# Kernel optimization log

Hardware: AMD Instinct MI355X
Metric: run time of the kernel (lower is better)

The kernel has to match this reference:

```python
import jax, jax.numpy as jnp
import numpy as np

TAU = 0.5      # init kwarg tau
LAMBD = 0.5    # init kwarg lambd
N, D, C = 4096, 1024, 512


def setup_inputs() -> dict:
    key = jax.random.key(0)
    k1, k2, k3 = jax.random.split(key, 3)
    return {
        "layer_embeds": jax.random.normal(k1, (N, D), dtype=jnp.float32),
        "y_true": jax.random.randint(k2, (N,), 0, C),
        "y_pred": jax.random.normal(k3, (N, C), dtype=jnp.float32),
    }


def _clce(x, y_true, y_pred):
    n = x.shape[0]
    # pairwise cosine similarity via one matmul (torch eps = 1e-8)
    norms = jnp.clip(jnp.linalg.norm(x, axis=1, keepdims=True), 1e-8)
    xn = x / norms
    sim = (xn @ xn.T + 1.0) * 0.5 * TAU          # [N, N]

    same = y_true[:, None] == y_true[None, :]    # diagonal is always True
    eye = jnp.eye(n, dtype=bool)
    pos_mask = same & ~eye                        # candidate positives (j != i)
    neg_mask = ~same                              # negatives (excludes diagonal)

    # slot 0: similarity to the FIRST positive j (in j order), else stays 0
    first_pos = jnp.argmax(pos_mask, axis=1)
    has_pos = pos_mask.any(axis=1)
    slot0 = jnp.where(has_pos,
                      jnp.take_along_axis(sim, first_pos[:, None], axis=1)[:, 0],
                      0.0)

    # negatives packed left-to-right into columns 1..; unfilled slots stay 0
    cum = jnp.cumsum(neg_mask, axis=1)            # 1-based slot per negative
    cols = jnp.where(neg_mask, cum, 2 * n - 1)    # non-negatives -> sink col
    rows = jnp.arange(n)[:, None]
    loss_temp = jnp.zeros((n, 2 * n), dtype=sim.dtype)
    loss_temp = loss_temp.at[rows, cols].add(jnp.where(neg_mask, sim, 0.0))
    loss_temp = loss_temp.at[:, 0].set(slot0)
    loss_temp = loss_temp[:, : 2 * n - 1]         # drop sink column -> [N, 2N-1]

    cl = -jax.nn.log_softmax(loss_temp, axis=1)[:, 0]
    cl = cl.sum() / n

    logp = jax.nn.log_softmax(y_pred, axis=1)
    ce = -jnp.take_along_axis(logp, y_true[:, None], axis=1).mean()

    return LAMBD * cl + (1.0 - LAMBD) * ce


def reference(layer_embeds, y_true, y_pred):
    return _clce(layer_embeds, y_true, y_pred)
```

## Files before the change

### kernel.cpp

```cpp
#include <hip/hip_runtime.h>
#include <hip/hip_bf16.h>

#define NR 4096
#define DIM 1024
#define NCLS 512

typedef __attribute__((ext_vector_type(4))) float f32x4;
typedef __attribute__((ext_vector_type(8))) short bf16x8;

static __device__ __forceinline__ unsigned short f2bf(float f) {
  __hip_bfloat16 h = __float2bfloat16(f);
  return *reinterpret_cast<unsigned short*>(&h);
}

__global__ __launch_bounds__(256) void k_prep(const float* __restrict__ x,
                                              const int* __restrict__ y,
                                              const float* __restrict__ yp,
                                              unsigned short* __restrict__ xn,
                                              int* __restrict__ cnt,
                                              int* __restrict__ fpos,
                                              float* __restrict__ slot0,
                                              float* __restrict__ ce,
                                              float* __restrict__ out) {
  const int b = blockIdx.x;
  const int tid = threadIdx.x;
  if (b < 1024) {
    int row = b * 4 + (tid >> 6);
    int lane = tid & 63;
    const float4* xr = reinterpret_cast<const float4*>(x + (size_t)row * DIM);
    float4 v[4];
    float s = 0.f;
#pragma unroll
    for (int it = 0; it < 4; ++it) {
      v[it] = xr[it * 64 + lane];
      s += v[it].x * v[it].x + v[it].y * v[it].y + v[it].z * v[it].z + v[it].w * v[it].w;
    }
#pragma unroll
    for (int d = 1; d < 64; d <<= 1) s += __shfl_xor(s, d);
    float inv = 1.0f / fmaxf(sqrtf(s), 1e-8f);
    ushort4* xo = reinterpret_cast<ushort4*>(xn + (size_t)row * DIM);
#pragma unroll
    for (int it = 0; it < 4; ++it) {
      ushort4 u;
      u.x = f2bf(v[it].x * inv);
      u.y = f2bf(v[it].y * inv);
      u.z = f2bf(v[it].z * inv);
      u.w = f2bf(v[it].w * inv);
      xo[it * 64 + lane] = u;
    }
  } else if (b < 2048) {
    int row = (b - 1024) * 4 + (tid >> 6);
    int lane = tid & 63;
    const float4* p = reinterpret_cast<const float4*>(yp + (size_t)row * NCLS);
    float4 v0 = p[lane], v1 = p[lane + 64];
    float m = fmaxf(fmaxf(fmaxf(v0.x, v0.y), fmaxf(v0.z, v0.w)),
                    fmaxf(fmaxf(v1.x, v1.y), fmaxf(v1.z, v1.w)));
#pragma unroll
    for (int d = 1; d < 64; d <<= 1) m = fmaxf(m, __shfl_xor(m, d));
    float s = __expf(v0.x - m) + __expf(v0.y - m) + __expf(v0.z - m) + __expf(v0.w - m) +
              __expf(v1.x - m) + __expf(v1.y - m) + __expf(v1.z - m) + __expf(v1.w - m);
#pragma unroll
    for (int d = 1; d < 64; d <<= 1) s += __shfl_xor(s, d);
    if (lane == 0) {
      float py = yp[(size_t)row * NCLS + y[row]];
      ce[row] = logf(s) + m - py;
    }
  } else {
    __shared__ int ys[NR];
    __shared__ int scnt[NCLS], sm1[NCLS], sm2[NCLS];
    for (int j = tid; j < NR; j += 256) ys[j] = y[j];
    for (int c = tid; c < NCLS; c += 256) { scnt[c] = 0; sm1[c] = NR; sm2[c] = NR; }
    __syncthreads();
    for (int i = tid; i < NR; i += 256) {
      int c = ys[i];
      atomicAdd(&scnt[c], 1);
      atomicMin(&sm1[c], i);
    }
    __syncthreads();
    for (int i = tid; i < NR; i += 256) {
      int c = ys[i];
      if (sm1[c] != i) atomicMin(&sm2[c], i);
    }
    __syncthreads();
    for (int i = tid; i < NR; i += 256) {
      int c = ys[i];
      int m1 = sm1[c];
      int j = (m1 == i) ? ((sm2[c] >= NR) ? -1 : sm2[c]) : m1;
      fpos[i] = j;
      slot0[i] = 0.f;
    }
    for (int c = tid; c < NCLS; c += 256) cnt[c] = scnt[c];
    if (tid == 0) out[0] = 0.f;
  }
}


#define STAGE(SSLOT, GROWBASE, KT)                                               \
  _Pragma("unroll") for (int q = 0; q < 2; ++q) {                                \
    const char* _src = (const char*)xn +                                         \
        (size_t)((GROWBASE) + srow[q]) * 2048 + (size_t)(KT) * 128 + scolb[q];   \
    __builtin_amdgcn_global_load_lds(                                            \
        (const __attribute__((address_space(1))) void*)_src,                     \
        (__attribute__((address_space(3))) void*)(lds + (SSLOT) + q * 8192 +     \
                                                  (w << 10)),                    \
        16, 0, 0);                                                               \
  }

#define PHASE(BUFB, MF0, LOADB, SSLOT, SBASE, SKT, VM)                           \
  {                                                                              \
    _Pragma("unroll") for (int mm = 0; mm < 2; ++mm)                             \
      _Pragma("unroll") for (int kk = 0; kk < 2; ++kk)                           \
        afr[mm][kk] = *(const bf16x8*)(lds + (BUFB) + ABaseW +                   \
                                       ((MF0) + mm) * 2048 + kk * 64 + kswz);    \
    if (LOADB) {                                                                 \
      _Pragma("unroll") for (int nf = 0; nf < 4; ++nf)                           \
        _Pragma("unroll") for (int kk = 0; kk < 2; ++kk)                         \
          bfr[nf][kk] = *(const bf16x8*)(lds + (BUFB) + BBaseW +                 \
                                         nf * 2048 + kk * 64 + kswz);            \
    }                                                                            \
    STAGE(SSLOT, SBASE, SKT)                                                     \
    if (VM) asm volatile("s_waitcnt vmcnt(4)" ::: "memory");                     \
    __builtin_amdgcn_s_barrier();                                                \
    asm volatile("s_waitcnt lgkmcnt(0)" ::: "memory");                           \
    __builtin_amdgcn_sched_barrier(0);                                           \
    __builtin_amdgcn_s_setprio(1);                                               \
    _Pragma("unroll") for (int kk = 0; kk < 2; ++kk)                             \
      _Pragma("unroll") for (int mm = 0; mm < 2; ++mm)                           \
        _Pragma("unroll") for (int nf = 0; nf < 4; ++nf)                         \
          acc[(MF0) + mm][nf] = __builtin_amdgcn_mfma_f32_16x16x32_bf16(         \
              afr[mm][kk], bfr[nf][kk], acc[(MF0) + mm][nf], 0, 0, 0);           \
    __builtin_amdgcn_s_setprio(0);                                               \
    __builtin_amdgcn_sched_barrier(0);                                           \
    __builtin_amdgcn_s_barrier();                                                \
  }

__global__ __launch_bounds__(512, 2) void k_gemm(const unsigned short* __restrict__ xn,
                                                 const int* __restrict__ y,
                                                 const int* __restrict__ fpos,
                                                 float* __restrict__ part,
                                                 float* __restrict__ slot0) {
  __shared__ char lds[131072];
  const int tid = threadIdx.x;
  const int w = tid >> 6, lane = tid & 63;
  const int wr = w >> 2, wcn = w & 3;
  const int r0 = lane & 15, klo = lane >> 4;

  const int bid = blockIdx.x;
  const int swzb = (bid & 7) * 32 + (bid >> 3);
  const int rb = swzb >> 4, cb = swzb & 15;
  const int rowbase = rb * 256, colbase = cb * 256;

  const int kswz = (klo * 16) ^ (((r0 >> 2) & 1) << 5);
  const int ABaseW = wr * 16384 + r0 * 128;
  const int BBaseW = 32768 + (wcn >> 1) * 16384 + (wcn & 1) * 8192 + r0 * 128;

  int srow[2], scolb[2];
#pragma unroll
  for (int q = 0; q < 2; ++q) {
    int D = q * 8192 + tid * 16;
    int L = D ^ (((D >> 9) & 1) << 5);
    srow[q] = L >> 7;
    scolb[q] = L & 127;
  }

  f32x4 acc[8][4] = {};

  STAGE(0, rowbase, 0)
  STAGE(16384, rowbase + 128, 0)
  STAGE(32768, colbase, 0)
  STAGE(49152, colbase + 128, 0)
  STAGE(65536 + 32768, colbase, 1)
  STAGE(65536 + 49152, colbase + 128, 1)
  asm volatile("s_waitcnt vmcnt(4)" ::: "memory");
  __builtin_amdgcn_s_barrier();

  for (int i = 0; i < 8; ++i) {
    const int t1 = 2 * i + 1;
    const int tn0 = (2 * i + 2 < 16) ? 2 * i + 2 : 15;
    const int tn1 = (2 * i + 3 < 16) ? 2 * i + 3 : 15;
    bf16x8 afr[2][2], bfr[4][2];
    PHASE(0, 0, 1, 65536, rowbase, t1, 0)
    PHASE(0, 2, 0, 65536 + 16384, rowbase + 128, t1, 0)
    PHASE(0, 4, 0, 32768, colbase, tn0, 0)
    PHASE(0, 6, 0, 49152, colbase + 128, tn0, 1)
    PHASE(65536, 0, 1, 0, rowbase, tn0, 0)
    PHASE(65536, 2, 0, 16384, rowbase + 128, tn0, 0)
    PHASE(65536, 4, 0, 65536 + 32768, colbase, tn1, 0)
    PHASE(65536, 6, 0, 65536 + 49152, colbase + 128, tn1, 1)
  }

  asm volatile("s_waitcnt vmcnt(0)" ::: "memory");
  __syncthreads();

  int* yrow_s = (int*)lds;
  int* ycol_s = (int*)(lds + 1024);
  int* frow_s = (int*)(lds + 2048);
  float* rsum = (float*)(lds + 4096);
  if (tid < 256) {
    yrow_s[tid] = y[rowbase + tid];
    frow_s[tid] = fpos[rowbase + tid];
  } else {
    ycol_s[tid - 256] = y[colbase + tid - 256];
  }
  __syncthreads();

  const int g = klo;
#pragma unroll
  for (int mf = 0; mf < 8; ++mf) {
    float rs[4] = {0.f, 0.f, 0.f, 0.f};
    int rloc[4], yr[4], fr[4];
#pragma unroll
    for (int reg = 0; reg < 4; ++reg) {
      rloc[reg] = wr * 128 + mf * 16 + g * 4 + reg;
      yr[reg] = yrow_s[rloc[reg]];
      fr[reg] = frow_s[rloc[reg]];
    }
#pragma unroll
    for (int nf = 0; nf < 4; ++nf) {
      int cl = wcn * 64 + nf * 16 + r0;
      int yc = ycol_s[cl];
      int gc = colbase + cl;
#pragma unroll
      for (int reg = 0; reg < 4; ++reg) {
        float sv = (acc[mf][nf][reg] + 1.0f) * 0.25f;
        float e = (yr[reg] == yc) ? 0.f : __expf(sv);
        rs[reg] += e;
        if (fr[reg] == gc) slot0[rowbase + rloc[reg]] = sv;
      }
    }
#pragma unroll
    for (int d = 1; d < 16; d <<= 1)
#pragma unroll
      for (int reg = 0; reg < 4; ++reg) rs[reg] += __shfl_xor(rs[reg], d);
    if (r0 == 0) {
#pragma unroll
      for (int reg = 0; reg < 4; ++reg)
        rsum[rloc[reg] * 4 + wcn] = rs[reg];
    }
  }
  __syncthreads();
  if (tid < 256)
    part[(size_t)cb * NR + rowbase + tid] =
        rsum[tid * 4] + rsum[tid * 4 + 1] + rsum[tid * 4 + 2] + rsum[tid * 4 + 3];
}

__global__ __launch_bounds__(256) void k_final(const float* __restrict__ part,
                                               const float* __restrict__ slot0,
                                               const int* __restrict__ cnt,
                                               const int* __restrict__ y,
                                               const float* __restrict__ ce,
                                               float* __restrict__ out) {
  __shared__ float red[256];
  const int tid = threadIdx.x;
  const int r = blockIdx.x * 256 + tid;
  float S = 0.f;
#pragma unroll
  for (int b = 0; b < 16; ++b) S += part[(size_t)b * NR + r];
  float s0 = slot0[r];
  float zeros = 4094.0f + (float)cnt[y[r]];
  float cl = logf(__expf(s0) + S + zeros) - s0;
  red[tid] = 0.5f * (cl + ce[r]);
  __syncthreads();
  for (int s = 128; s > 0; s >>= 1) {
    if (tid < s) red[tid] += red[tid + s];
    __syncthreads();
  }
  if (tid == 0) atomicAdd(out, red[0] / (float)NR);
}

extern "C" void kernel_launch(void* const* d_in, const int* in_sizes, int n_in,
                              void* d_out, int out_size, void* d_ws, size_t ws_size,
                              hipStream_t stream) {
  const float* x = (const float*)d_in[0];
  const int* y = (const int*)d_in[1];
  const float* yp = (const float*)d_in[2];
  float* out = (float*)d_out;

  char* w = (char*)d_ws;
  unsigned short* xn = (unsigned short*)w;
  int* cnt = (int*)(w + 8388608);
  int* fpos = (int*)(w + 8390656);
  float* slot0 = (float*)(w + 8407040);
  float* part = (float*)(w + 8423424);
  float* ce = (float*)(w + 8685568);

  k_prep<<<2049, 256, 0, stream>>>(x, y, yp, xn, cnt, fpos, slot0, ce, out);
  k_gemm<<<256, 512, 0, stream>>>(xn, y, fpos, part, slot0);
  k_final<<<16, 256, 0, stream>>>(part, slot0, cnt, y, ce, out);
}
```

Measured before the change: 55.37 us.

## Switch Gram matrix GEMM from bf16 to scaled fp8 e4m3 MFMA

The normalized embeddings are quantized to fp8 e4m3 with a scale of 64 and stored in a k-permuted layout, so the GEMM can use 16x16x32 fp8 MFMA and rescale the accumulator by 1/4096 in the epilogue. This halves the global traffic and LDS footprint (128KB to 64KB) and reduces staging loads per phase. It risks accuracy, since cosine similarities computed from fp8 inputs carry much larger rounding error than bf16, and the packed layout and swizzle must line up exactly with the MFMA operand order.

New measurement: 49.10 us. 1.13x faster.

```diff
diff --git a/kernel.cpp b/kernel.cpp
--- a/kernel.cpp
+++ b/kernel.cpp
@@ -1,22 +1,18 @@
 #include <hip/hip_runtime.h>
 #include <hip/hip_bf16.h>
+#include <hip/hip_fp8.h>
 
 #define NR 4096
 #define DIM 1024
 #define NCLS 512
 
 typedef __attribute__((ext_vector_type(4))) float f32x4;
-typedef __attribute__((ext_vector_type(8))) short bf16x8;
-
-static __device__ __forceinline__ unsigned short f2bf(float f) {
-  __hip_bfloat16 h = __float2bfloat16(f);
-  return *reinterpret_cast<unsigned short*>(&h);
-}
+typedef __attribute__((ext_vector_type(2))) long i64x2;
 
 __global__ __launch_bounds__(256) void k_prep(const float* __restrict__ x,
                                               const int* __restrict__ y,
                                               const float* __restrict__ yp,
-                                              unsigned short* __restrict__ xn,
+                                              unsigned char* __restrict__ xnp,
                                               int* __restrict__ cnt,
                                               int* __restrict__ fpos,
                                               float* __restrict__ slot0,
@@ -37,16 +33,19 @@
     }
 #pragma unroll
     for (int d = 1; d < 64; d <<= 1) s += __shfl_xor(s, d);
-    float inv = 1.0f / fmaxf(sqrtf(s), 1e-8f);
-    ushort4* xo = reinterpret_cast<ushort4*>(xn + (size_t)row * DIM);
+    float inv = 64.0f / fmaxf(sqrtf(s), 1e-8f);
+    unsigned char* xo = xnp + (size_t)row * DIM;
 #pragma unroll
     for (int it = 0; it < 4; ++it) {
-      ushort4 u;
-      u.x = f2bf(v[it].x * inv);
-      u.y = f2bf(v[it].y * inv);
-      u.z = f2bf(v[it].z * inv);
-      u.w = f2bf(v[it].w * inv);
-      xo[it * 64 + lane] = u;
+      int k0q = it * 64 + lane;
+      int kt = k0q >> 4;
+      int r6 = (k0q & 15) * 4;
+      int p = ((r6 & 31) >> 3) * 16 + (r6 >> 5) * 8 + (r6 & 7);
+      __hip_fp8_e4m3 b0(v[it].x * inv), b1(v[it].y * inv),
+                     b2(v[it].z * inv), b3(v[it].w * inv);
+      unsigned int pk = (unsigned int)b0.__x | ((unsigned int)b1.__x << 8) |
+                        ((unsigned int)b2.__x << 16) | ((unsigned int)b3.__x << 24);
+      *(unsigned int*)(xo + kt * 64 + p) = pk;
     }
   } else if (b < 2048) {
     int row = (b - 1024) * 4 + (tid >> 6);
@@ -96,30 +95,26 @@
 
 
 #define STAGE(SSLOT, GROWBASE, KT)                                               \
-  _Pragma("unroll") for (int q = 0; q < 2; ++q) {                                \
-    const char* _src = (const char*)xn +                                         \
-        (size_t)((GROWBASE) + srow[q]) * 2048 + (size_t)(KT) * 128 + scolb[q];   \
+  {                                                                              \
+    const char* _src = (const char*)xnp +                                        \
+        (size_t)((GROWBASE) + srow) * 1024 + (size_t)(KT) * 64 + scol;           \
     __builtin_amdgcn_global_load_lds(                                            \
         (const __attribute__((address_space(1))) void*)_src,                     \
-        (__attribute__((address_space(3))) void*)(lds + (SSLOT) + q * 8192 +     \
-                                                  (w << 10)),                    \
+        (__attribute__((address_space(3))) void*)(lds + (SSLOT) + (w << 10)),    \
         16, 0, 0);                                                               \
   }
 
 #define PHASE(BUFB, MF0, LOADB, SSLOT, SBASE, SKT, VM)                           \
   {                                                                              \
     _Pragma("unroll") for (int mm = 0; mm < 2; ++mm)                             \
-      _Pragma("unroll") for (int kk = 0; kk < 2; ++kk)                           \
-        afr[mm][kk] = *(const bf16x8*)(lds + (BUFB) + ABaseW +                   \
-                                       ((MF0) + mm) * 2048 + kk * 64 + kswz);    \
+      afr[mm] = *(const i64x2*)(lds + (BUFB) + ABaseW +                          \
+                                ((MF0) + mm) * 1024 + kread);                    \
     if (LOADB) {                                                                 \
       _Pragma("unroll") for (int nf = 0; nf < 4; ++nf)                           \
-        _Pragma("unroll") for (int kk = 0; kk < 2; ++kk)                         \
-          bfr[nf][kk] = *(const bf16x8*)(lds + (BUFB) + BBaseW +                 \
-                                         nf * 2048 + kk * 64 + kswz);            \
+        bfr[nf] = *(const i64x2*)(lds + (BUFB) + BBaseW + nf * 1024 + kread);    \
     }                                                                            \
     STAGE(SSLOT, SBASE, SKT)                                                     \
-    if (VM) asm volatile("s_waitcnt vmcnt(4)" ::: "memory");                     \
+    if (VM) asm volatile("s_waitcnt vmcnt(2)" ::: "memory");                     \
     __builtin_amdgcn_s_barrier();                                                \
     asm volatile("s_waitcnt lgkmcnt(0)" ::: "memory");                           \
     __builtin_amdgcn_sched_barrier(0);                                           \
@@ -127,19 +122,19 @@
     _Pragma("unroll") for (int kk = 0; kk < 2; ++kk)                             \
       _Pragma("unroll") for (int mm = 0; mm < 2; ++mm)                           \
         _Pragma("unroll") for (int nf = 0; nf < 4; ++nf)                         \
-          acc[(MF0) + mm][nf] = __builtin_amdgcn_mfma_f32_16x16x32_bf16(         \
+          acc[(MF0) + mm][nf] = __builtin_amdgcn_mfma_f32_16x16x32_fp8_fp8(      \
               afr[mm][kk], bfr[nf][kk], acc[(MF0) + mm][nf], 0, 0, 0);           \
     __builtin_amdgcn_s_setprio(0);                                               \
     __builtin_amdgcn_sched_barrier(0);                                           \
     __builtin_amdgcn_s_barrier();                                                \
   }
 
-__global__ __launch_bounds__(512, 2) void k_gemm(const unsigned short* __restrict__ xn,
+__global__ __launch_bounds__(512, 2) void k_gemm(const unsigned char* __restrict__ xnp,
                                                  const int* __restrict__ y,
                                                  const int* __restrict__ fpos,
                                                  float* __restrict__ part,
                                                  float* __restrict__ slot0) {
-  __shared__ char lds[131072];
+  __shared__ char lds[65536];
   const int tid = threadIdx.x;
   const int w = tid >> 6, lane = tid & 63;
   const int wr = w >> 2, wcn = w & 3;
@@ -150,43 +145,42 @@
   const int rb = swzb >> 4, cb = swzb & 15;
   const int rowbase = rb * 256, colbase = cb * 256;
 
-  const int kswz = (klo * 16) ^ (((r0 >> 2) & 1) << 5);
-  const int ABaseW = wr * 16384 + r0 * 128;
-  const int BBaseW = 32768 + (wcn >> 1) * 16384 + (wcn & 1) * 8192 + r0 * 128;
-
-  int srow[2], scolb[2];
-#pragma unroll
-  for (int q = 0; q < 2; ++q) {
-    int D = q * 8192 + tid * 16;
-    int L = D ^ (((D >> 9) & 1) << 5);
-    srow[q] = L >> 7;
-    scolb[q] = L & 127;
+  const int kread = (klo * 16) ^ ((r0 & 3) << 4);
+  const int ABaseW = wr * 8192 + r0 * 64;
+  const int BBaseW = 16384 + (wcn >> 1) * 8192 + (wcn & 1) * 4096 + r0 * 64;
+
+  int srow, scol;
+  {
+    int D = tid * 16;
+    int L = D ^ (((D >> 6) & 3) << 4);
+    srow = L >> 6;
+    scol = L & 63;
   }
 
   f32x4 acc[8][4] = {};
 
   STAGE(0, rowbase, 0)
-  STAGE(16384, rowbase + 128, 0)
-  STAGE(32768, colbase, 0)
-  STAGE(49152, colbase + 128, 0)
-  STAGE(65536 + 32768, colbase, 1)
-  STAGE(65536 + 49152, colbase + 128, 1)
-  asm volatile("s_waitcnt vmcnt(4)" ::: "memory");
+  STAGE(8192, rowbase + 128, 0)
+  STAGE(16384, colbase, 0)
+  STAGE(24576, colbase + 128, 0)
+  STAGE(32768 + 16384, colbase, 1)
+  STAGE(32768 + 24576, colbase + 128, 1)
+  asm volatile("s_waitcnt vmcnt(2)" ::: "memory");
   __builtin_amdgcn_s_barrier();
 
   for (int i = 0; i < 8; ++i) {
     const int t1 = 2 * i + 1;
     const int tn0 = (2 * i + 2 < 16) ? 2 * i + 2 : 15;
     const int tn1 = (2 * i + 3 < 16) ? 2 * i + 3 : 15;
-    bf16x8 afr[2][2], bfr[4][2];
-    PHASE(0, 0, 1, 65536, rowbase, t1, 0)
-    PHASE(0, 2, 0, 65536 + 16384, rowbase + 128, t1, 0)
-    PHASE(0, 4, 0, 32768, colbase, tn0, 0)
-    PHASE(0, 6, 0, 49152, colbase + 128, tn0, 1)
-    PHASE(65536, 0, 1, 0, rowbase, tn0, 0)
-    PHASE(65536, 2, 0, 16384, rowbase + 128, tn0, 0)
-    PHASE(65536, 4, 0, 65536 + 32768, colbase, tn1, 0)
-    PHASE(65536, 6, 0, 65536 + 49152, colbase + 128, tn1, 1)
+    i64x2 afr[2], bfr[4];
+    PHASE(0, 0, 1, 32768, rowbase, t1, 0)
+    PHASE(0, 2, 0, 32768 + 8192, rowbase + 128, t1, 0)
+    PHASE(0, 4, 0, 16384, colbase, tn0, 0)
+    PHASE(0, 6, 0, 24576, colbase + 128, tn0, 1)
+    PHASE(32768, 0, 1, 0, rowbase, tn0, 0)
+    PHASE(32768, 2, 0, 8192, rowbase + 128, tn0, 0)
+    PHASE(32768, 4, 0, 32768 + 16384, colbase, tn1, 0)
+    PHASE(32768, 6, 0, 32768 + 24576, colbase + 128, tn1, 1)
   }
 
   asm volatile("s_waitcnt vmcnt(0)" ::: "memory");
@@ -222,7 +216,7 @@
       int gc = colbase + cl;
 #pragma unroll
       for (int reg = 0; reg < 4; ++reg) {
-        float sv = (acc[mf][nf][reg] + 1.0f) * 0.25f;
+        float sv = acc[mf][nf][reg] * (1.0f / 16384.f) + 0.25f;
         float e = (yr[reg] == yc) ? 0.f : __expf(sv);
         rs[reg] += e;
         if (fr[reg] == gc) slot0[rowbase + rloc[reg]] = sv;
@@ -277,14 +271,14 @@
   float* out = (float*)d_out;
 
   char* w = (char*)d_ws;
-  unsigned short* xn = (unsigned short*)w;
-  int* cnt = (int*)(w + 8388608);
-  int* fpos = (int*)(w + 8390656);
-  float* slot0 = (float*)(w + 8407040);
-  float* part = (float*)(w + 8423424);
-  float* ce = (float*)(w + 8685568);
-
-  k_prep<<<2049, 256, 0, stream>>>(x, y, yp, xn, cnt, fpos, slot0, ce, out);
-  k_gemm<<<256, 512, 0, stream>>>(xn, y, fpos, part, slot0);
+  unsigned char* xnp = (unsigned char*)w;
+  int* cnt = (int*)(w + 4194304);
+  int* fpos = (int*)(w + 4196352);
+  float* slot0 = (float*)(w + 4212736);
+  float* part = (float*)(w + 4229120);
+  float* ce = (float*)(w + 4491264);
+
+  k_prep<<<2049, 256, 0, stream>>>(x, y, yp, xnp, cnt, fpos, slot0, ce, out);
+  k_gemm<<<256, 512, 0, stream>>>(xnp, y, fpos, part, slot0);
   k_final<<<16, 256, 0, stream>>>(part, slot0, cnt, y, ce, out);
 }
```
